# Kernel optimization log

Hardware: AMD Instinct MI355X
Metric: run time of the kernel (lower is better)

Reference implementation:

```python
import jax, jax.numpy as jnp
import numpy as np

IN_FEATURES = 2048
OUT_FEATURES = 8192


def setup_inputs() -> dict:
    key = jax.random.key(0)
    k_x, k_w, k_s, k_b = jax.random.split(key, 4)
    x = jax.random.normal(k_x, (4, 2048, IN_FEATURES), dtype=jnp.float32)
    # int8 weights as produced by quantize(): values in [-128, 127]
    weight_int8 = jax.random.randint(k_w, (OUT_FEATURES, IN_FEATURES), -128, 128, dtype=jnp.int8)
    # per-output-row scale, shape [out_features, 1]
    scale = jax.random.uniform(k_s, (OUT_FEATURES, 1), dtype=jnp.float32, minval=1e-4, maxval=0.02)
    bias = jax.random.normal(k_b, (OUT_FEATURES,), dtype=jnp.float32) * 0.01
    return {"x": x, "weight_int8": weight_int8, "scale": scale, "bias": bias}


def reference(x, weight_int8, scale, bias):
    # dequantize: [out, in] int8 -> x.dtype, scaled per output row
    weight = weight_int8.astype(x.dtype) * scale.astype(x.dtype)
    # F.linear: x @ weight.T + bias
    return jnp.einsum('bsi,oi->bso', x, weight) + bias.astype(x.dtype)
```

## Files before the change

kernel.cpp:

```cpp
#include <hip/hip_runtime.h>
#include <hip/hip_bf16.h>

#define M_DIM 8192
#define N_DIM 8192
#define K_DIM 2048

#define BK 64
#define NT (K_DIM / BK)
#define SLOT_BYTES 16384

typedef float f32x4 __attribute__((ext_vector_type(4)));
typedef int   i32x4 __attribute__((ext_vector_type(4)));
typedef unsigned int u32;
typedef u32 u32x2 __attribute__((ext_vector_type(2)));
typedef u32 u32x4 __attribute__((ext_vector_type(4)));


__device__ __forceinline__ void gload16(const unsigned char* g, char* l) {
    __builtin_amdgcn_global_load_lds(
        (const __attribute__((address_space(1))) u32*)g,
        (__attribute__((address_space(3))) u32*)l, 16, 0, 0);
}

__device__ __forceinline__ u32 pack4(int a, int b, int c, int d) {
    return (u32)(a & 255) | ((u32)(b & 255) << 8) |
           ((u32)(c & 255) << 16) | ((u32)(d & 255) << 24);
}


__global__ void __launch_bounds__(256) quant_x_k(const float* __restrict__ x,
                                                 unsigned char* __restrict__ xq,
                                                 float* __restrict__ sx) {
    const int row = blockIdx.x;
    const int t = threadIdx.x;
    const float* xr = x + (size_t)row * K_DIM;
    f32x4 v0 = *((const f32x4*)xr + t * 2);
    f32x4 v1 = *((const f32x4*)xr + t * 2 + 1);
    float m = fabsf(v0[0]);
    m = fmaxf(m, fabsf(v0[1])); m = fmaxf(m, fabsf(v0[2])); m = fmaxf(m, fabsf(v0[3]));
    m = fmaxf(m, fabsf(v1[0])); m = fmaxf(m, fabsf(v1[1]));
    m = fmaxf(m, fabsf(v1[2])); m = fmaxf(m, fabsf(v1[3]));
#pragma unroll
    for (int off = 32; off >= 1; off >>= 1)
        m = fmaxf(m, __shfl_xor(m, off, 64));
    __shared__ float wmax[4];
    if ((t & 63) == 0) wmax[t >> 6] = m;
    __syncthreads();
    m = fmaxf(fmaxf(wmax[0], wmax[1]), fmaxf(wmax[2], wmax[3]));
    m = fmaxf(m, 1e-20f);
    const float rs = 127.0f / m;
    const int q0 = (int)rintf(v0[0] * rs), q1 = (int)rintf(v0[1] * rs);
    const int q2 = (int)rintf(v0[2] * rs), q3 = (int)rintf(v0[3] * rs);
    const int q4 = (int)rintf(v1[0] * rs), q5 = (int)rintf(v1[1] * rs);
    const int q6 = (int)rintf(v1[2] * rs), q7 = (int)rintf(v1[3] * rs);
    u32x2 o;
    o[0] = pack4(q0, q1, q2, q3);
    o[1] = pack4(q4, q5, q6, q7);
    *((u32x2*)(xq + (size_t)row * K_DIM) + t) = o;
    if (t == 0) sx[row] = m / 127.0f;
}


__global__ void __launch_bounds__(256) cvt_w_k(const int* __restrict__ w,
                                               unsigned char* __restrict__ wq, int n16) {
    const int stride = gridDim.x * blockDim.x;
    for (int i = blockIdx.x * blockDim.x + threadIdx.x; i < n16; i += stride) {
        const i32x4* p = (const i32x4*)w + (size_t)i * 4;
        i32x4 a = p[0], b = p[1], c = p[2], d = p[3];
        u32x4 o;
        o[0] = pack4(a[0], a[1], a[2], a[3]);
        o[1] = pack4(b[0], b[1], b[2], b[3]);
        o[2] = pack4(c[0], c[1], c[2], c[3]);
        o[3] = pack4(d[0], d[1], d[2], d[3]);
        *((u32x4*)wq + i) = o;
    }
}


__global__ void __launch_bounds__(512, 2)
gemm_i8(const unsigned char* __restrict__ Aq, const unsigned char* __restrict__ Bq,
        const float* __restrict__ sx, const float* __restrict__ sw,
        const float* __restrict__ bias, float* __restrict__ C) {
    extern __shared__ __align__(16) char ldsb[];

    const int bid = blockIdx.x;
    const int swz = (bid & 7) * 128 + (bid >> 3);
    const int rowBase = (swz >> 5) * 256;
    const int colBase = (swz & 31) * 256;

    const int t = threadIdx.x;
    const int l = t & 63;
    const int w = t >> 6;
    const int wm = w >> 2;
    const int wn = w & 3;
    const int fr = l & 15;
    const int s4 = l >> 4;

    const int sr = t >> 2;
    const int sk = (((t & 3) ^ ((sr >> 1) & 3)) * 16);
    const unsigned char* gA0 = Aq + (size_t)(rowBase + sr) * K_DIM + sk;
    const unsigned char* gA1 = Aq + (size_t)(rowBase + 128 + sr) * K_DIM + sk;

#define STAGE_A(tk) do { \
        char* _b = ldsb + ((tk) & 3) * SLOT_BYTES; \
        const int _k = (tk) * BK; \
        gload16(gA0 + _k, _b + t * 16); \
        gload16(gA1 + _k, _b + 8192 + t * 16); \
    } while (0)

    const unsigned char* gBf = Bq + (size_t)(colBase + wn * 64 + fr) * K_DIM + s4 * 16;

#define BLOAD(dst, tk) do { \
        const unsigned char* _g = gBf + (size_t)(tk) * BK; \
        _Pragma("unroll") \
        for (int ni = 0; ni < 4; ++ni) \
            dst[ni] = *(const i32x4*)(_g + (size_t)ni * 16 * K_DIM); \
    } while (0)

    const int pc = ((s4 ^ ((fr >> 1) & 3)) * 16);
    int aoff[8];
#pragma unroll
    for (int mi = 0; mi < 8; ++mi)
        aoff[mi] = (wm * 128 + mi * 16 + fr) * 64 + pc;

    i32x4 acc[8][4] = {};
    i32x4 afC[8], bf0[4], bf1[4];

#define SB    __builtin_amdgcn_sched_barrier(0)
#define BAR   __builtin_amdgcn_s_barrier()
#define P1    __builtin_amdgcn_s_setprio(1)
#define P0    __builtin_amdgcn_s_setprio(0)
#define LGKM0 asm volatile("s_waitcnt lgkmcnt(0)" ::: "memory")
#define VM6   asm volatile("s_waitcnt vmcnt(6)" ::: "memory")
#define VM4   asm volatile("s_waitcnt vmcnt(4)" ::: "memory")
#define VM2   asm volatile("s_waitcnt vmcnt(2)" ::: "memory")
#define VM0   asm volatile("s_waitcnt vmcnt(0)" ::: "memory")

#define READS_A(tk) do { \
        const char* _s = ldsb + ((tk) & 3) * SLOT_BYTES; \
        _Pragma("unroll") \
        for (int mi = 0; mi < 8; ++mi) afC[mi] = *(const i32x4*)(_s + aoff[mi]); \
    } while (0)

#define MFMA_ILV(BREG, NTK) do { P1; \
        const char* _n = ldsb + ((NTK) & 3) * SLOT_BYTES; \
        _Pragma("unroll") \
        for (int mi = 0; mi < 8; ++mi) { \
            _Pragma("unroll") \
            for (int ni = 0; ni < 4; ++ni) \
                acc[mi][ni] = __builtin_amdgcn_mfma_i32_16x16x64_i8( \
                    afC[mi], BREG[ni], acc[mi][ni], 0, 0, 0); \
            afC[mi] = *(const i32x4*)(_n + aoff[mi]); \
        } \
        P0; } while (0)

#define MFMA_ALL(BREG) do { P1; \
        _Pragma("unroll") \
        for (int mi = 0; mi < 8; ++mi) \
            _Pragma("unroll") \
            for (int ni = 0; ni < 4; ++ni) \
                acc[mi][ni] = __builtin_amdgcn_mfma_i32_16x16x64_i8( \
                    afC[mi], BREG[ni], acc[mi][ni], 0, 0, 0); \
        P0; } while (0)

#define BODY(TK, BCUR, BNXT) do { \
        STAGE_A((TK) + 3); \
        BLOAD(BNXT, (TK) + 1); \
        VM6; LGKM0; SB; BAR; SB; \
        MFMA_ILV(BCUR, (TK) + 1); \
    } while (0)

    STAGE_A(0); STAGE_A(1);
    BLOAD(bf0, 0);
    STAGE_A(2);
    VM2; SB; BAR; SB;
    READS_A(0);

#pragma unroll 1
    for (int tk = 0; tk < NT - 4; tk += 2) {
        BODY(tk, bf0, bf1);
        BODY(tk + 1, bf1, bf0);
    }
    BODY(28, bf0, bf1);
    BLOAD(bf0, 30);
    VM4; LGKM0; SB; BAR; SB;
    MFMA_ILV(bf1, 30);
    BLOAD(bf1, 31);
    VM4; LGKM0; SB; BAR; SB;
    MFMA_ILV(bf0, 31);
    VM0; LGKM0; SB;
    MFMA_ALL(bf1);

#undef BODY
#undef MFMA_ALL
#undef MFMA_ILV
#undef READS_A
#undef BLOAD
#undef STAGE_A

#pragma unroll
    for (int ni = 0; ni < 4; ++ni) {
        const int col = colBase + wn * 64 + ni * 16 + fr;
        const float swc = sw[col];
        const float bz = bias[col];
#pragma unroll
        for (int mi = 0; mi < 8; ++mi) {
            const int rb = rowBase + wm * 128 + mi * 16 + s4 * 4;
            i32x4 a = acc[mi][ni];
#pragma unroll
            for (int r = 0; r < 4; ++r)
                C[(size_t)(rb + r) * N_DIM + col] =
                    (float)a[r] * (sx[rb + r] * swc) + bz;
        }
    }
}


typedef int i32x4_t __attribute__((ext_vector_type(4)));
__global__ void __launch_bounds__(256) naive_k(const float* __restrict__ x,
                                               const int* __restrict__ w,
                                               const float* __restrict__ scale,
                                               const float* __restrict__ bias,
                                               float* __restrict__ out) {
    __shared__ float xs[K_DIM];
    const int m = blockIdx.x >> 5;
    const int n = ((blockIdx.x & 31) << 8) + threadIdx.x;
    for (int i = threadIdx.x; i < K_DIM; i += 256) xs[i] = x[(size_t)m * K_DIM + i];
    __syncthreads();
    const int* wr = w + (size_t)n * K_DIM;
    float acc = 0.f;
    for (int k = 0; k < K_DIM; k += 4) {
        i32x4_t v = *(const i32x4_t*)(wr + k);
        acc += xs[k]     * (float)v[0];
        acc += xs[k + 1] * (float)v[1];
        acc += xs[k + 2] * (float)v[2];
        acc += xs[k + 3] * (float)v[3];
    }
    out[(size_t)m * N_DIM + n] = acc * scale[n] + bias[n];
}


extern "C" void kernel_launch(void* const* d_in, const int* in_sizes, int n_in,
                              void* d_out, int out_size, void* d_ws, size_t ws_size,
                              hipStream_t stream) {
    const float* x     = (const float*)d_in[0];
    const int*   w8    = (const int*)d_in[1];
    const float* sw    = (const float*)d_in[2];
    const float* bias  = (const float*)d_in[3];
    float*       out   = (float*)d_out;

    const size_t xq_bytes = (size_t)M_DIM * K_DIM;
    const size_t wq_bytes = (size_t)N_DIM * K_DIM;
    const size_t need = xq_bytes + wq_bytes + (size_t)M_DIM * sizeof(float);
    if (ws_size >= need) {
        unsigned char* xq = (unsigned char*)d_ws;
        unsigned char* wq = xq + xq_bytes;
        float* sx = (float*)(wq + wq_bytes);
        hipFuncSetAttribute((const void*)gemm_i8,
                            hipFuncAttributeMaxDynamicSharedMemorySize, 65536);
        quant_x_k<<<M_DIM, 256, 0, stream>>>(x, xq, sx);
        cvt_w_k<<<2048, 256, 0, stream>>>(w8, wq, N_DIM * K_DIM / 16);
        gemm_i8<<<dim3((M_DIM / 256) * (N_DIM / 256)), 512, 65536, stream>>>(
            xq, wq, sx, sw, bias, out);
    } else {
        naive_k<<<(M_DIM * (N_DIM / 256)), 256, 0, stream>>>(x, w8, sw, bias, out);
    }
}
```

Before: 247.2 us.

## Pre-tile int8 weights into fragment-contiguous layout for coalesced B loads

```diff
diff --git a/kernel.cpp b/kernel.cpp
--- a/kernel.cpp
+++ b/kernel.cpp
@@ -49,36 +49,43 @@
     m = fmaxf(fmaxf(wmax[0], wmax[1]), fmaxf(wmax[2], wmax[3]));
     m = fmaxf(m, 1e-20f);
     const float rs = 127.0f / m;
-    const int q0 = (int)rintf(v0[0] * rs), q1 = (int)rintf(v0[1] * rs);
-    const int q2 = (int)rintf(v0[2] * rs), q3 = (int)rintf(v0[3] * rs);
-    const int q4 = (int)rintf(v1[0] * rs), q5 = (int)rintf(v1[1] * rs);
-    const int q6 = (int)rintf(v1[2] * rs), q7 = (int)rintf(v1[3] * rs);
     u32x2 o;
-    o[0] = pack4(q0, q1, q2, q3);
-    o[1] = pack4(q4, q5, q6, q7);
+    o[0] = pack4((int)rintf(v0[0] * rs), (int)rintf(v0[1] * rs),
+                 (int)rintf(v0[2] * rs), (int)rintf(v0[3] * rs));
+    o[1] = pack4((int)rintf(v1[0] * rs), (int)rintf(v1[1] * rs),
+                 (int)rintf(v1[2] * rs), (int)rintf(v1[3] * rs));
     *((u32x2*)(xq + (size_t)row * K_DIM) + t) = o;
     if (t == 0) sx[row] = m / 127.0f;
 }
 
 
 __global__ void __launch_bounds__(256) cvt_w_k(const int* __restrict__ w,
-                                               unsigned char* __restrict__ wq, int n16) {
-    const int stride = gridDim.x * blockDim.x;
-    for (int i = blockIdx.x * blockDim.x + threadIdx.x; i < n16; i += stride) {
-        const i32x4* p = (const i32x4*)w + (size_t)i * 4;
-        i32x4 a = p[0], b = p[1], c = p[2], d = p[3];
+                                               unsigned char* __restrict__ Bt) {
+    const int g = blockIdx.x;
+    const int t = threadIdx.x;
+    const int fr = t >> 4;
+    const int kc = t & 15;
+    const int col = g * 16 + fr;
+    const int* wr = w + (size_t)col * K_DIM + kc * 128;
+
+#pragma unroll
+    for (int kk = 0; kk < 8; ++kk) {
+        const int k = kc * 128 + kk * 16;
+        const int kt = k >> 6;
+        const int s4 = (k >> 4) & 3;
         u32x4 o;
-        o[0] = pack4(a[0], a[1], a[2], a[3]);
-        o[1] = pack4(b[0], b[1], b[2], b[3]);
-        o[2] = pack4(c[0], c[1], c[2], c[3]);
-        o[3] = pack4(d[0], d[1], d[2], d[3]);
-        *((u32x4*)wq + i) = o;
+#pragma unroll
+        for (int j = 0; j < 4; ++j) {
+            i32x4 a = *(const i32x4*)(wr + kk * 16 + j * 4);
+            o[j] = pack4(a[0], a[1], a[2], a[3]);
+        }
+        *(u32x4*)(Bt + (size_t)g * 32768 + kt * 1024 + (s4 * 16 + fr) * 16) = o;
     }
 }
 
 
 __global__ void __launch_bounds__(512, 2)
-gemm_i8(const unsigned char* __restrict__ Aq, const unsigned char* __restrict__ Bq,
+gemm_i8(const unsigned char* __restrict__ Aq, const unsigned char* __restrict__ Bt,
         const float* __restrict__ sx, const float* __restrict__ sw,
         const float* __restrict__ bias, float* __restrict__ C) {
     extern __shared__ __align__(16) char ldsb[];
@@ -108,13 +115,15 @@
         gload16(gA1 + _k, _b + 8192 + t * 16); \
     } while (0)
 
-    const unsigned char* gBf = Bq + (size_t)(colBase + wn * 64 + fr) * K_DIM + s4 * 16;
-
-#define BLOAD(dst, tk) do { \
-        const unsigned char* _g = gBf + (size_t)(tk) * BK; \
+    const unsigned char* bB[4];
+#pragma unroll
+    for (int ni = 0; ni < 4; ++ni)
+        bB[ni] = Bt + (size_t)(colBase / 16 + wn * 4 + ni) * 32768 + l * 16;
+
+#define BLOAD(dst, T) do { \
         _Pragma("unroll") \
         for (int ni = 0; ni < 4; ++ni) \
-            dst[ni] = *(const i32x4*)(_g + (size_t)ni * 16 * K_DIM); \
+            dst[ni] = *(const i32x4*)(bB[ni] + (T) * 1024); \
     } while (0)
 
     const int pc = ((s4 ^ ((fr >> 1) & 3)) * 16);
@@ -129,11 +138,10 @@
 #define SB    __builtin_amdgcn_sched_barrier(0)
 #define BAR   __builtin_amdgcn_s_barrier()
 #define P1    __builtin_amdgcn_s_setprio(1)
-#define P0    __builtin_amdgcn_s_setprio(0)
+#define P0p   __builtin_amdgcn_s_setprio(0)
 #define LGKM0 asm volatile("s_waitcnt lgkmcnt(0)" ::: "memory")
 #define VM6   asm volatile("s_waitcnt vmcnt(6)" ::: "memory")
 #define VM4   asm volatile("s_waitcnt vmcnt(4)" ::: "memory")
-#define VM2   asm volatile("s_waitcnt vmcnt(2)" ::: "memory")
 #define VM0   asm volatile("s_waitcnt vmcnt(0)" ::: "memory")
 
 #define READS_A(tk) do { \
@@ -152,7 +160,7 @@
                     afC[mi], BREG[ni], acc[mi][ni], 0, 0, 0); \
             afC[mi] = *(const i32x4*)(_n + aoff[mi]); \
         } \
-        P0; } while (0)
+        P0p; } while (0)
 
 #define MFMA_ALL(BREG) do { P1; \
         _Pragma("unroll") \
@@ -161,33 +169,28 @@
             for (int ni = 0; ni < 4; ++ni) \
                 acc[mi][ni] = __builtin_amdgcn_mfma_i32_16x16x64_i8( \
                     afC[mi], BREG[ni], acc[mi][ni], 0, 0, 0); \
-        P0; } while (0)
-
-#define BODY(TK, BCUR, BNXT) do { \
-        STAGE_A((TK) + 3); \
-        BLOAD(BNXT, (TK) + 1); \
-        VM6; LGKM0; SB; BAR; SB; \
-        MFMA_ILV(BCUR, (TK) + 1); \
-    } while (0)
-
-    STAGE_A(0); STAGE_A(1);
+        P0p; } while (0)
+
+#define BODY(T, BCUR, BNXT, DOSTG, VMW) do { \
+        BLOAD(BNXT, (T) + 1); \
+        if (DOSTG) STAGE_A((T) + 3); \
+        VMW; LGKM0; SB; BAR; SB; \
+        MFMA_ILV(BCUR, (T) + 1); \
+    } while (0)
+
+    STAGE_A(0); STAGE_A(1); STAGE_A(2);
     BLOAD(bf0, 0);
-    STAGE_A(2);
-    VM2; SB; BAR; SB;
+    VM4; SB; BAR; SB;
     READS_A(0);
 
+    BODY(0, bf0, bf1, true, VM6);
 #pragma unroll 1
-    for (int tk = 0; tk < NT - 4; tk += 2) {
-        BODY(tk, bf0, bf1);
-        BODY(tk + 1, bf1, bf0);
-    }
-    BODY(28, bf0, bf1);
-    BLOAD(bf0, 30);
-    VM4; LGKM0; SB; BAR; SB;
-    MFMA_ILV(bf1, 30);
-    BLOAD(bf1, 31);
-    VM4; LGKM0; SB; BAR; SB;
-    MFMA_ILV(bf0, 31);
+    for (int T = 1; T <= 27; T += 2) {
+        BODY(T,     bf1, bf0, true, VM6);
+        BODY(T + 1, bf0, bf1, true, VM6);
+    }
+    BODY(29, bf1, bf0, false, VM6);
+    BODY(30, bf0, bf1, false, VM4);
     VM0; LGKM0; SB;
     MFMA_ALL(bf1);
 
@@ -254,14 +257,14 @@
     const size_t need = xq_bytes + wq_bytes + (size_t)M_DIM * sizeof(float);
     if (ws_size >= need) {
         unsigned char* xq = (unsigned char*)d_ws;
-        unsigned char* wq = xq + xq_bytes;
-        float* sx = (float*)(wq + wq_bytes);
+        unsigned char* Bt = xq + xq_bytes;
+        float* sx = (float*)(Bt + wq_bytes);
         hipFuncSetAttribute((const void*)gemm_i8,
                             hipFuncAttributeMaxDynamicSharedMemorySize, 65536);
         quant_x_k<<<M_DIM, 256, 0, stream>>>(x, xq, sx);
-        cvt_w_k<<<2048, 256, 0, stream>>>(w8, wq, N_DIM * K_DIM / 16);
+        cvt_w_k<<<N_DIM / 16, 256, 0, stream>>>(w8, Bt);
         gemm_i8<<<dim3((M_DIM / 256) * (N_DIM / 256)), 512, 65536, stream>>>(
-            xq, wq, sx, sw, bias, out);
+            xq, Bt, sx, sw, bias, out);
     } else {
         naive_k<<<(M_DIM * (N_DIM / 256)), 256, 0, stream>>>(x, w8, sw, bias, out);
     }
```

Result: faster. 218.9 us (-11.5%).
